# Kernel tuning notes

Measured on AMD Instinct MI355X. Metric: run time of the kernel, lower is better.

The kernel has to match this reference:

```python
import jax, jax.numpy as jnp
import numpy as np

N_NODES = 50000
N_EDGES = 800000
IN_FEAT = 4
HIDDEN = 128
NUM_LAYERS = 3


def setup_inputs() -> dict:
    key = jax.random.key(0)
    ks = jax.random.split(key, 16)
    x = jax.random.normal(ks[0], (N_NODES, IN_FEAT), dtype=jnp.float32)
    edge_index = jax.random.randint(ks[1], (2, N_EDGES), 0, N_NODES, dtype=jnp.int64)

    def lin(k, fan_in, fan_out):
        bound = 1.0 / np.sqrt(fan_in)
        k1, k2 = jax.random.split(k)
        W = jax.random.uniform(k1, (fan_in, fan_out), minval=-bound, maxval=bound, dtype=jnp.float32)
        b = jax.random.uniform(k2, (fan_out,), minval=-bound, maxval=bound, dtype=jnp.float32)
        return W, b

    W_enc, b_enc = lin(ks[2], IN_FEAT, HIDDEN)
    W_g1, b_g1 = lin(ks[3], HIDDEN, HIDDEN)
    W_g2, b_g2 = lin(ks[4], HIDDEN, HIDDEN)
    W_g3, b_g3 = lin(ks[5], HIDDEN, HIDDEN)
    W_m1, b_m1 = lin(ks[6], 2 * HIDDEN, HIDDEN)
    W_m2, b_m2 = lin(ks[7], HIDDEN, 3)
    return {
        "x": x, "edge_index": edge_index,
        "W_enc": W_enc, "b_enc": b_enc,
        "W_g1": W_g1, "b_g1": b_g1,
        "W_g2": W_g2, "b_g2": b_g2,
        "W_g3": W_g3, "b_g3": b_g3,
        "W_m1": W_m1, "b_m1": b_m1,
        "W_m2": W_m2, "b_m2": b_m2,
    }


def _gcn_forward(x, edge_index, W_enc, b_enc, gcn_params, W_m1, b_m1, W_m2, b_m2):
    n = x.shape[0]
    # Node encoder (linear + ReLU) -> [N, H]
    h = jax.nn.relu(x @ W_enc + b_enc)

    # Add self-loops once (GCNConv default add_self_loops=True)
    src = jnp.concatenate([edge_index[0], jnp.arange(n, dtype=edge_index.dtype)])
    dst = jnp.concatenate([edge_index[1], jnp.arange(n, dtype=edge_index.dtype)])
    # Symmetric degree normalization: D^{-1/2} (A+I) D^{-1/2}
    deg = jax.ops.segment_sum(jnp.ones_like(dst, dtype=h.dtype), dst, num_segments=n)
    deg_inv_sqrt = jnp.where(deg > 0, jax.lax.rsqrt(jnp.maximum(deg, 1.0)), 0.0)
    norm = (deg_inv_sqrt[src] * deg_inv_sqrt[dst])[:, None]  # [E+N, 1]

    for (W, b) in gcn_params:
        m = (h @ W)[src] * norm                       # gather + scale messages
        h = jax.ops.segment_sum(m, dst, num_segments=n) + b
        h = jax.nn.relu(h)                            # dropout is identity at eval

    # Edge classifier: gather endpoints, concat, MLP -> [E, 3]
    ef = jnp.concatenate([h[edge_index[0]], h[edge_index[1]]], axis=-1)
    return jax.nn.relu(ef @ W_m1 + b_m1) @ W_m2 + b_m2


def reference(x, edge_index, W_enc, b_enc, W_g1, b_g1, W_g2, b_g2, W_g3, b_g3, W_m1, b_m1, W_m2, b_m2):
    gcn_params = [(W_g1, b_g1), (W_g2, b_g2), (W_g3, b_g3)]
    return _gcn_forward(x, edge_index, W_enc, b_enc, gcn_params, W_m1, b_m1, W_m2, b_m2)
```

## Files before the change

### kernel.cpp

```cpp
#include <hip/hip_runtime.h>
#include <hip/hip_bf16.h>

#define N_NODES 50000
#define N_EDGES 800000
#define HID 128
#define SCAN_BLK 512
#define N_SCAN_BLOCKS ((N_NODES + SCAN_BLK - 1) / SCAN_BLK)

typedef __attribute__((ext_vector_type(8))) short bf16x8;
typedef __attribute__((ext_vector_type(4))) float f32x4;

__device__ __forceinline__ ushort f2bf(float f) {
    uint u = __float_as_uint(f);
    return (ushort)((u + 0x7FFFu + ((u >> 16) & 1u)) >> 16);
}
__device__ __forceinline__ float bf2f(ushort h) { return __uint_as_float(((uint)h) << 16); }

__global__ void k_count(const int* __restrict__ ei, int* cnt) {
    int e = blockIdx.x * blockDim.x + threadIdx.x;
    if (e < N_EDGES) atomicAdd(&cnt[ei[N_EDGES + e]], 1);
}

__global__ __launch_bounds__(SCAN_BLK) void k_scan1(const int* __restrict__ cnt,
                                                    int* __restrict__ rowStart,
                                                    int* __restrict__ blockSums,
                                                    float* __restrict__ dinv) {
    __shared__ int tmp[SCAN_BLK];
    int i = blockIdx.x * SCAN_BLK + threadIdx.x;
    int v = (i < N_NODES) ? cnt[i] : 0;
    if (i < N_NODES) dinv[i] = rsqrtf(1.0f + (float)v);
    tmp[threadIdx.x] = v;
    __syncthreads();
    for (int off = 1; off < SCAN_BLK; off <<= 1) {
        int t = (threadIdx.x >= off) ? tmp[threadIdx.x - off] : 0;
        __syncthreads();
        tmp[threadIdx.x] += t;
        __syncthreads();
    }
    if (i < N_NODES) rowStart[i] = tmp[threadIdx.x] - v;
    if (threadIdx.x == SCAN_BLK - 1) blockSums[blockIdx.x] = tmp[SCAN_BLK - 1];
}

__global__ __launch_bounds__(SCAN_BLK) void k_scan23(int* __restrict__ rowStart,
                                                     const int* __restrict__ blockSums,
                                                     int* __restrict__ cursor) {
    __shared__ int ps[128];
    int t = threadIdx.x;
    if (t < 128) ps[t] = (t < N_SCAN_BLOCKS) ? blockSums[t] : 0;
    __syncthreads();
    for (int off = 1; off < 128; off <<= 1) {
        int v = (t < 128 && t >= off) ? ps[t - off] : 0;
        __syncthreads();
        if (t < 128) ps[t] += v;
        __syncthreads();
    }
    int i = blockIdx.x * SCAN_BLK + t;
    int prefix = (blockIdx.x == 0) ? 0 : ps[blockIdx.x - 1];
    if (i < N_NODES) {
        rowStart[i] += prefix;
        cursor[i] = 0;
    }
    if (i == 0) rowStart[N_NODES] = N_EDGES;
}

__global__ void k_fill(const int* __restrict__ ei, const int* __restrict__ rowStart,
                       int* cursor, int2* __restrict__ csrE) {
    int e = blockIdx.x * blockDim.x + threadIdx.x;
    if (e < N_EDGES) {
        int s = ei[e];
        int d = ei[N_EDGES + e];
        int pos = rowStart[d] + atomicAdd(&cursor[d], 1);
        csrE[pos] = make_int2(s, e);
    }
}

struct WSplitArgs {
    const float* src[5];
    ushort* th[5];
    ushort* tl[5];
};

__global__ void k_tsplit5(WSplitArgs a) {
    int i = blockIdx.x * 256 + threadIdx.x;
    int which = i >> 14, r = i & 16383;
    int k = r >> 7, j = r & 127;
    float v = a.src[which][r];
    ushort hi = f2bf(v);
    a.th[which][j * 128 + k] = hi;
    a.tl[which][j * 128 + k] = f2bf(v - bf2f(hi));
}

__global__ void k_encoder(const float* __restrict__ x, const float* __restrict__ W,
                          const float* __restrict__ b, ushort* __restrict__ hH,
                          ushort* __restrict__ hL) {
    int i = blockIdx.x * 256 + threadIdx.x;
    int n = i >> 6, l = i & 63;
    int j = l * 2;
    float4 xv = *(const float4*)(x + (size_t)n * 4);
    float2 acc = *(const float2*)(b + j);
    float2 w0 = *(const float2*)(W + 0 * 128 + j);
    float2 w1 = *(const float2*)(W + 1 * 128 + j);
    float2 w2 = *(const float2*)(W + 2 * 128 + j);
    float2 w3 = *(const float2*)(W + 3 * 128 + j);
    acc.x += xv.x * w0.x + xv.y * w1.x + xv.z * w2.x + xv.w * w3.x;
    acc.y += xv.x * w0.y + xv.y * w1.y + xv.z * w2.y + xv.w * w3.y;
    float v0 = fmaxf(acc.x, 0.f), v1 = fmaxf(acc.y, 0.f);
    ushort h0 = f2bf(v0), h1 = f2bf(v1);
    ushort l0 = f2bf(v0 - bf2f(h0)), l1 = f2bf(v1 - bf2f(h1));
    ((uint*)hH)[i] = (uint)h0 | ((uint)h1 << 16);
    ((uint*)hL)[i] = (uint)l0 | ((uint)l1 << 16);
}

__global__ __launch_bounds__(256) void k_gemm_mfma(const ushort* __restrict__ AH,
                                                   const ushort* __restrict__ AL,
                                                   const ushort* __restrict__ BTH,
                                                   const ushort* __restrict__ BTL,
                                                   float* __restrict__ out,
                                                   const float* __restrict__ scale, int M) {
    int tid = threadIdx.x;
    int w = tid >> 6, l = tid & 63;
    int ln = l & 15, lk = l >> 4;
    int r0 = blockIdx.x * 128 + w * 32;
    int row0 = r0 + ln, row1 = r0 + 16 + ln;
    int a0 = row0 < M ? row0 : M - 1;
    int a1 = row1 < M ? row1 : M - 1;

    f32x4 acc0[8] = {};
    f32x4 acc1[8] = {};
#pragma unroll
    for (int kc = 0; kc < 4; ++kc) {
        int ko = kc * 32 + lk * 8;
        bf16x8 h0H = *(const bf16x8*)(AH + (size_t)a0 * 128 + ko);
        bf16x8 h0L = *(const bf16x8*)(AL + (size_t)a0 * 128 + ko);
        bf16x8 h1H = *(const bf16x8*)(AH + (size_t)a1 * 128 + ko);
        bf16x8 h1L = *(const bf16x8*)(AL + (size_t)a1 * 128 + ko);
#pragma unroll
        for (int nt = 0; nt < 8; ++nt) {
            size_t boff = (size_t)(nt * 16 + ln) * 128 + ko;
            bf16x8 wH = *(const bf16x8*)(BTH + boff);
            bf16x8 wL = *(const bf16x8*)(BTL + boff);
            acc0[nt] = __builtin_amdgcn_mfma_f32_16x16x32_bf16(wH, h0H, acc0[nt], 0, 0, 0);
            acc0[nt] = __builtin_amdgcn_mfma_f32_16x16x32_bf16(wL, h0H, acc0[nt], 0, 0, 0);
            acc0[nt] = __builtin_amdgcn_mfma_f32_16x16x32_bf16(wH, h0L, acc0[nt], 0, 0, 0);
            acc1[nt] = __builtin_amdgcn_mfma_f32_16x16x32_bf16(wH, h1H, acc1[nt], 0, 0, 0);
            acc1[nt] = __builtin_amdgcn_mfma_f32_16x16x32_bf16(wL, h1H, acc1[nt], 0, 0, 0);
            acc1[nt] = __builtin_amdgcn_mfma_f32_16x16x32_bf16(wH, h1L, acc1[nt], 0, 0, 0);
        }
    }
    float s0v = scale[a0];
    float s1v = scale[a1];
#pragma unroll
    for (int nt = 0; nt < 8; ++nt) {
        int jb = nt * 16 + lk * 4;
        if (row0 < M) {
            float4 o = make_float4(acc0[nt][0] * s0v, acc0[nt][1] * s0v,
                                   acc0[nt][2] * s0v, acc0[nt][3] * s0v);
            *(float4*)(out + (size_t)row0 * 128 + jb) = o;
        }
        if (row1 < M) {
            float4 o = make_float4(acc1[nt][0] * s1v, acc1[nt][1] * s1v,
                                   acc1[nt][2] * s1v, acc1[nt][3] * s1v);
            *(float4*)(out + (size_t)row1 * 128 + jb) = o;
        }
    }
}

__global__ __launch_bounds__(512, 8) void k_agg_gemm(
    const float* __restrict__ hw, const float* __restrict__ bg,
    const float* __restrict__ dinv, const int* __restrict__ rowStart,
    const int2* __restrict__ csrE,
    const ushort* __restrict__ BTH1, const ushort* __restrict__ BTL1,
    const ushort* __restrict__ BTH2, const ushort* __restrict__ BTL2,
    float* __restrict__ out1, float* __restrict__ out2,
    const float* __restrict__ b1, const float* __restrict__ outScale) {
    __shared__ uint AsH[16][64];
    __shared__ uint AsL[16][64];
    int tid = threadIdx.x;
    int w = tid >> 6, l = tid & 63;
    int g = l >> 4, li = l & 15;
    int c8 = li * 8;

#pragma unroll
    for (int q = 0; q < 2; ++q) {
        int n = blockIdx.x * 16 + w * 2 + q;
        float4 aA, aB;
        if (g == 0) {
            aA = *(const float4*)(hw + (size_t)n * 128 + c8);
            aB = *(const float4*)(hw + (size_t)n * 128 + c8 + 4);
        } else {
            aA = make_float4(0.f, 0.f, 0.f, 0.f);
            aB = aA;
        }
        int s0 = rowStart[n], s1 = rowStart[n + 1];
        int k = s0 + g;
        float4 v0a = make_float4(0.f, 0.f, 0.f, 0.f), v0b = v0a;
        if (k < s1) {
            const float* r = hw + (size_t)csrE[k].x * 128 + c8;
            v0a = *(const float4*)(r);
            v0b = *(const float4*)(r + 4);
        }
        for (; k < s1; k += 4) {
            float4 v1a = make_float4(0.f, 0.f, 0.f, 0.f), v1b = v1a;
            if (k + 4 < s1) {
                const float* r = hw + (size_t)csrE[k + 4].x * 128 + c8;
                v1a = *(const float4*)(r);
                v1b = *(const float4*)(r + 4);
            }
            aA.x += v0a.x; aA.y += v0a.y; aA.z += v0a.z; aA.w += v0a.w;
            aB.x += v0b.x; aB.y += v0b.y; aB.z += v0b.z; aB.w += v0b.w;
            v0a = v1a;
            v0b = v1b;
        }
        aA.x += __shfl_xor(aA.x, 16); aA.y += __shfl_xor(aA.y, 16);
        aA.z += __shfl_xor(aA.z, 16); aA.w += __shfl_xor(aA.w, 16);
        aB.x += __shfl_xor(aB.x, 16); aB.y += __shfl_xor(aB.y, 16);
        aB.z += __shfl_xor(aB.z, 16); aB.w += __shfl_xor(aB.w, 16);
        aA.x += __shfl_xor(aA.x, 32); aA.y += __shfl_xor(aA.y, 32);
        aA.z += __shfl_xor(aA.z, 32); aA.w += __shfl_xor(aA.w, 32);
        aB.x += __shfl_xor(aB.x, 32); aB.y += __shfl_xor(aB.y, 32);
        aB.z += __shfl_xor(aB.z, 32); aB.w += __shfl_xor(aB.w, 32);

        if (g == 0) {
            float di = dinv[n];
            float4 bbA = *(const float4*)(bg + c8);
            float4 bbB = *(const float4*)(bg + c8 + 4);
            float f0 = fmaxf(bbA.x + di * aA.x, 0.f);
            float f1 = fmaxf(bbA.y + di * aA.y, 0.f);
            float f2 = fmaxf(bbA.z + di * aA.z, 0.f);
            float f3 = fmaxf(bbA.w + di * aA.w, 0.f);
            float f4 = fmaxf(bbB.x + di * aB.x, 0.f);
            float f5 = fmaxf(bbB.y + di * aB.y, 0.f);
            float f6 = fmaxf(bbB.z + di * aB.z, 0.f);
            float f7 = fmaxf(bbB.w + di * aB.w, 0.f);
            ushort h0 = f2bf(f0), h1 = f2bf(f1), h2 = f2bf(f2), h3 = f2bf(f3);
            ushort h4 = f2bf(f4), h5 = f2bf(f5), h6 = f2bf(f6), h7 = f2bf(f7);
            uint4 uh = make_uint4((uint)h0 | ((uint)h1 << 16), (uint)h2 | ((uint)h3 << 16),
                                  (uint)h4 | ((uint)h5 << 16), (uint)h6 | ((uint)h7 << 16));
            ushort l0 = f2bf(f0 - bf2f(h0)), l1 = f2bf(f1 - bf2f(h1));
            ushort l2 = f2bf(f2 - bf2f(h2)), l3 = f2bf(f3 - bf2f(h3));
            ushort l4 = f2bf(f4 - bf2f(h4)), l5 = f2bf(f5 - bf2f(h5));
            ushort l6 = f2bf(f6 - bf2f(h6)), l7 = f2bf(f7 - bf2f(h7));
            uint4 ul = make_uint4((uint)l0 | ((uint)l1 << 16), (uint)l2 | ((uint)l3 << 16),
                                  (uint)l4 | ((uint)l5 << 16), (uint)l6 | ((uint)l7 << 16));
            int r = w * 2 + q;
            *(uint4*)&AsH[r][li * 4] = uh;
            *(uint4*)&AsL[r][li * 4] = ul;
        }
    }
    __syncthreads();

    int ln = l & 15, lk = l >> 4;
    int ct = w;
    int node = blockIdx.x * 16 + ln;
    f32x4 acc1 = {};
    f32x4 acc2 = {};
#pragma unroll
    for (int kc = 0; kc < 4; ++kc) {
        uint4 uh = *(uint4*)&AsH[ln][kc * 16 + lk * 4];
        uint4 ul = *(uint4*)&AsL[ln][kc * 16 + lk * 4];
        bf16x8 hh, hl;
        __builtin_memcpy(&hh, &uh, 16);
        __builtin_memcpy(&hl, &ul, 16);
        size_t boff = (size_t)(ct * 16 + ln) * 128 + kc * 32 + lk * 8;
        bf16x8 wh = *(const bf16x8*)(BTH1 + boff);
        bf16x8 wl = *(const bf16x8*)(BTL1 + boff);
        acc1 = __builtin_amdgcn_mfma_f32_16x16x32_bf16(wh, hh, acc1, 0, 0, 0);
        acc1 = __builtin_amdgcn_mfma_f32_16x16x32_bf16(wl, hh, acc1, 0, 0, 0);
        acc1 = __builtin_amdgcn_mfma_f32_16x16x32_bf16(wh, hl, acc1, 0, 0, 0);
        if (BTH2) {
            bf16x8 wh2 = *(const bf16x8*)(BTH2 + boff);
            bf16x8 wl2 = *(const bf16x8*)(BTL2 + boff);
            acc2 = __builtin_amdgcn_mfma_f32_16x16x32_bf16(wh2, hh, acc2, 0, 0, 0);
            acc2 = __builtin_amdgcn_mfma_f32_16x16x32_bf16(wl2, hh, acc2, 0, 0, 0);
            acc2 = __builtin_amdgcn_mfma_f32_16x16x32_bf16(wh2, hl, acc2, 0, 0, 0);
        }
    }
    int jb = ct * 16 + lk * 4;
    if (outScale) {
        float s = outScale[node];
        *(float4*)(out1 + (size_t)node * 128 + jb) =
            make_float4(acc1[0] * s, acc1[1] * s, acc1[2] * s, acc1[3] * s);
    } else {
        *(float4*)(out1 + (size_t)node * 128 + jb) =
            make_float4(acc1[0], acc1[1], acc1[2], acc1[3]);
        float4 bv = *(const float4*)(b1 + jb);
        *(float4*)(out2 + (size_t)node * 128 + jb) =
            make_float4(acc2[0] + bv.x, acc2[1] + bv.y, acc2[2] + bv.z, acc2[3] + bv.w);
    }
}

__global__ __launch_bounds__(256) void k_edge_final(const float* __restrict__ P,
                                                    const float* __restrict__ Qb,
                                                    const int* __restrict__ rowStart,
                                                    const int2* __restrict__ csrE,
                                                    const float* __restrict__ W2,
                                                    const float* __restrict__ b2,
                                                    float* __restrict__ out) {
    int wid = (blockIdx.x * 256 + threadIdx.x) >> 6;
    int l = threadIdx.x & 63;
    if (wid >= N_NODES) return;
    int s0 = rowStart[wid], s1 = rowStart[wid + 1];
    if (s0 >= s1) return;
    int j8 = (l & 15) * 8;
    int g = l >> 4;

    float4 qa = *(const float4*)(Qb + (size_t)wid * 128 + j8);
    float4 qb = *(const float4*)(Qb + (size_t)wid * 128 + j8 + 4);
    float w2r[8][3];
#pragma unroll
    for (int k = 0; k < 8; ++k) {
        w2r[k][0] = W2[(j8 + k) * 3 + 0];
        w2r[k][1] = W2[(j8 + k) * 3 + 1];
        w2r[k][2] = W2[(j8 + k) * 3 + 2];
    }
    float bz0 = b2[0], bz1 = b2[1], bz2 = b2[2];

    int k = s0 + g;
    int2 c = make_int2(0, 0);
    float4 pa = make_float4(0.f, 0.f, 0.f, 0.f), pb = pa;
    if (k < s1) {
        c = csrE[k];
        const float* pr = P + (size_t)c.x * 128 + j8;
        pa = *(const float4*)(pr);
        pb = *(const float4*)(pr + 4);
    }
    for (; k < s1; k += 4) {
        int kn = k + 4;
        int2 cn = make_int2(0, 0);
        float4 pan = make_float4(0.f, 0.f, 0.f, 0.f), pbn = pan;
        if (kn < s1) {
            cn = csrE[kn];
            const float* prn = P + (size_t)cn.x * 128 + j8;
            pan = *(const float4*)(prn);
            pbn = *(const float4*)(prn + 4);
        }
        float z[8];
        z[0] = fmaxf(pa.x + qa.x, 0.f);
        z[1] = fmaxf(pa.y + qa.y, 0.f);
        z[2] = fmaxf(pa.z + qa.z, 0.f);
        z[3] = fmaxf(pa.w + qa.w, 0.f);
        z[4] = fmaxf(pb.x + qb.x, 0.f);
        z[5] = fmaxf(pb.y + qb.y, 0.f);
        z[6] = fmaxf(pb.z + qb.z, 0.f);
        z[7] = fmaxf(pb.w + qb.w, 0.f);
        float o0 = 0.f, o1 = 0.f, o2 = 0.f;
#pragma unroll
        for (int q = 0; q < 8; ++q) {
            o0 += z[q] * w2r[q][0];
            o1 += z[q] * w2r[q][1];
            o2 += z[q] * w2r[q][2];
        }
#pragma unroll
        for (int m = 1; m < 16; m <<= 1) {
            o0 += __shfl_xor(o0, m);
            o1 += __shfl_xor(o1, m);
            o2 += __shfl_xor(o2, m);
        }
        if ((l & 15) == 0) {
            float* op = out + (size_t)c.y * 3;
            op[0] = o0 + bz0;
            op[1] = o1 + bz1;
            op[2] = o2 + bz2;
        }
        c = cn;
        pa = pan;
        pb = pbn;
    }
}

extern "C" void kernel_launch(void* const* d_in, const int* in_sizes, int n_in,
                              void* d_out, int out_size, void* d_ws, size_t ws_size,
                              hipStream_t stream) {
    const float* x     = (const float*)d_in[0];
    const int*   ei    = (const int*)d_in[1];
    const float* W_enc = (const float*)d_in[2];
    const float* b_enc = (const float*)d_in[3];
    const float* Wg[3] = {(const float*)d_in[4], (const float*)d_in[6], (const float*)d_in[8]};
    const float* bg[3] = {(const float*)d_in[5], (const float*)d_in[7], (const float*)d_in[9]};
    const float* W_m1  = (const float*)d_in[10];
    const float* b_m1  = (const float*)d_in[11];
    const float* W_m2  = (const float*)d_in[12];
    const float* b_m2  = (const float*)d_in[13];
    float* out = (float*)d_out;

    char* w = (char*)d_ws;
    ushort* hH      = (ushort*)w;  w += (size_t)N_NODES * HID * 2;
    ushort* hL      = (ushort*)w;  w += (size_t)N_NODES * HID * 2;
    float*  bufA    = (float*)w;   w += (size_t)N_NODES * HID * 4;
    float*  bufB    = (float*)w;   w += (size_t)N_NODES * HID * 4;
    int2*   csrE    = (int2*)w;    w += (size_t)N_EDGES * 8;
    float*  dinv    = (float*)w;   w += (size_t)N_NODES * 4;
    int*    rowStart= (int*)w;     w += (size_t)(N_NODES + 4) * 4;
    int*    cursor  = (int*)w;     w += (size_t)N_NODES * 4;
    int*    blockSums=(int*)w;     w += 512;
    ushort* WgTH[3], *WgTL[3];
    for (int i = 0; i < 3; ++i) {
        WgTH[i] = (ushort*)w; w += 128 * 128 * 2;
        WgTL[i] = (ushort*)w; w += 128 * 128 * 2;
    }
    ushort* WtTH = (ushort*)w; w += 128 * 128 * 2;
    ushort* WtTL = (ushort*)w; w += 128 * 128 * 2;
    ushort* WbTH = (ushort*)w; w += 128 * 128 * 2;
    ushort* WbTL = (ushort*)w; w += 128 * 128 * 2;

    float* P  = (float*)hH;
    float* Qb = bufB;

    hipMemsetAsync(cursor, 0, (size_t)N_NODES * 4, stream);
    k_count<<<(N_EDGES + 255) / 256, 256, 0, stream>>>(ei, cursor);
    k_scan1<<<N_SCAN_BLOCKS, SCAN_BLK, 0, stream>>>(cursor, rowStart, blockSums, dinv);
    k_scan23<<<N_SCAN_BLOCKS, SCAN_BLK, 0, stream>>>(rowStart, blockSums, cursor);
    k_fill<<<(N_EDGES + 255) / 256, 256, 0, stream>>>(ei, rowStart, cursor, csrE);

    WSplitArgs wa;
    wa.src[0] = Wg[0]; wa.th[0] = WgTH[0]; wa.tl[0] = WgTL[0];
    wa.src[1] = Wg[1]; wa.th[1] = WgTH[1]; wa.tl[1] = WgTL[1];
    wa.src[2] = Wg[2]; wa.th[2] = WgTH[2]; wa.tl[2] = WgTL[2];
    wa.src[3] = W_m1;             wa.th[3] = WtTH; wa.tl[3] = WtTL;
    wa.src[4] = W_m1 + 128 * 128; wa.th[4] = WbTH; wa.tl[4] = WbTL;
    k_tsplit5<<<5 * 16384 / 256, 256, 0, stream>>>(wa);

    k_encoder<<<N_NODES * 64 / 256, 256, 0, stream>>>(x, W_enc, b_enc, hH, hL);

    k_gemm_mfma<<<(N_NODES + 127) / 128, 256, 0, stream>>>(hH, hL, WgTH[0], WgTL[0], bufA, dinv, N_NODES);

    const int fusedGrid = N_NODES / 16;
    k_agg_gemm<<<fusedGrid, 512, 0, stream>>>(bufA, bg[0], dinv, rowStart, csrE,
                                              WgTH[1], WgTL[1], nullptr, nullptr,
                                              bufB, nullptr, nullptr, dinv);
    k_agg_gemm<<<fusedGrid, 512, 0, stream>>>(bufB, bg[1], dinv, rowStart, csrE,
                                              WgTH[2], WgTL[2], nullptr, nullptr,
                                              bufA, nullptr, nullptr, dinv);
    k_agg_gemm<<<fusedGrid, 512, 0, stream>>>(bufA, bg[2], dinv, rowStart, csrE,
                                              WtTH, WtTL, WbTH, WbTL,
                                              P, Qb, b_m1, nullptr);

    k_edge_final<<<(N_NODES * 64) / 256, 256, 0, stream>>>(P, Qb, rowStart, csrE, W_m2, b_m2, out);
}
```

Before: 477.3 us.

## Renumber nodes by in-degree so aggregation blocks get balanced neighbor counts

Replaces the CSR prefix scan with a degree-bucket histogram and ranking pass that permutes nodes so that consecutive nodes have equal in-degree. The encoder writes features in permuted order, and the CSR stores permuted source indices. The aggregation kernel now gives two nodes to each wavefront, using half-waves of two lanes per feature group, and pads the shared-memory rows to avoid bank conflicts. The goal is less wavefront divergence and load imbalance from uneven degrees during the gather loops. The cost is extra preprocessing kernels, and the locality of the random gathers changes. The final edge output still appears to be indexed by the original edge id.

```diff
diff --git a/kernel.cpp b/kernel.cpp
--- a/kernel.cpp
+++ b/kernel.cpp
@@ -4,8 +4,8 @@
 #define N_NODES 50000
 #define N_EDGES 800000
 #define HID 128
-#define SCAN_BLK 512
-#define N_SCAN_BLOCKS ((N_NODES + SCAN_BLK - 1) / SCAN_BLK)
+#define NBUCKET 1024
+#define N_NODE_BLOCKS ((N_NODES + 255) / 256)
 
 typedef __attribute__((ext_vector_type(8))) short bf16x8;
 typedef __attribute__((ext_vector_type(4))) float f32x4;
@@ -21,56 +21,80 @@
     if (e < N_EDGES) atomicAdd(&cnt[ei[N_EDGES + e]], 1);
 }
 
-__global__ __launch_bounds__(SCAN_BLK) void k_scan1(const int* __restrict__ cnt,
-                                                    int* __restrict__ rowStart,
-                                                    int* __restrict__ blockSums,
-                                                    float* __restrict__ dinv) {
-    __shared__ int tmp[SCAN_BLK];
-    int i = blockIdx.x * SCAN_BLK + threadIdx.x;
-    int v = (i < N_NODES) ? cnt[i] : 0;
-    if (i < N_NODES) dinv[i] = rsqrtf(1.0f + (float)v);
-    tmp[threadIdx.x] = v;
+__global__ __launch_bounds__(256) void k_bhist(const int* __restrict__ cnt, int* gHist,
+                                               int* __restrict__ blockBase) {
+    __shared__ int lh[NBUCKET];
+    int t = threadIdx.x;
+    for (int d = t; d < NBUCKET; d += 256) lh[d] = 0;
     __syncthreads();
-    for (int off = 1; off < SCAN_BLK; off <<= 1) {
-        int t = (threadIdx.x >= off) ? tmp[threadIdx.x - off] : 0;
+    int n = blockIdx.x * 256 + t;
+    if (n < N_NODES) {
+        int deg = min(cnt[n], NBUCKET - 1);
+        atomicAdd(&lh[deg], 1);
+    }
+    __syncthreads();
+    for (int d = t; d < NBUCKET; d += 256) {
+        int c = lh[d];
+        blockBase[blockIdx.x * NBUCKET + d] = c ? atomicAdd(&gHist[d], c) : 0;
+    }
+}
+
+__global__ __launch_bounds__(NBUCKET) void k_prefix(const int* __restrict__ gHist,
+                                                    int* __restrict__ histBase,
+                                                    int* __restrict__ edgeBase,
+                                                    int* __restrict__ rowStartP) {
+    __shared__ int a[NBUCKET];
+    __shared__ int b[NBUCKET];
+    int t = threadIdx.x;
+    int h = gHist[t];
+    a[t] = h;
+    b[t] = h * t;
+    __syncthreads();
+    for (int off = 1; off < NBUCKET; off <<= 1) {
+        int av = (t >= off) ? a[t - off] : 0;
+        int bv = (t >= off) ? b[t - off] : 0;
         __syncthreads();
-        tmp[threadIdx.x] += t;
+        a[t] += av;
+        b[t] += bv;
         __syncthreads();
     }
-    if (i < N_NODES) rowStart[i] = tmp[threadIdx.x] - v;
-    if (threadIdx.x == SCAN_BLK - 1) blockSums[blockIdx.x] = tmp[SCAN_BLK - 1];
-}
-
-__global__ __launch_bounds__(SCAN_BLK) void k_scan23(int* __restrict__ rowStart,
-                                                     const int* __restrict__ blockSums,
-                                                     int* __restrict__ cursor) {
-    __shared__ int ps[128];
+    histBase[t] = a[t] - h;
+    edgeBase[t] = b[t] - h * t;
+    if (t == 0) rowStartP[N_NODES] = N_EDGES;
+}
+
+__global__ __launch_bounds__(256) void k_rank(const int* __restrict__ cnt,
+                                              const int* __restrict__ histBase,
+                                              const int* __restrict__ edgeBase,
+                                              const int* __restrict__ blockBase,
+                                              int* __restrict__ rank,
+                                              int* __restrict__ rowStartP,
+                                              float* __restrict__ dinvP) {
+    __shared__ int cur[NBUCKET];
     int t = threadIdx.x;
-    if (t < 128) ps[t] = (t < N_SCAN_BLOCKS) ? blockSums[t] : 0;
+    for (int d = t; d < NBUCKET; d += 256) cur[d] = 0;
     __syncthreads();
-    for (int off = 1; off < 128; off <<= 1) {
-        int v = (t < 128 && t >= off) ? ps[t - off] : 0;
-        __syncthreads();
-        if (t < 128) ps[t] += v;
-        __syncthreads();
-    }
-    int i = blockIdx.x * SCAN_BLK + t;
-    int prefix = (blockIdx.x == 0) ? 0 : ps[blockIdx.x - 1];
-    if (i < N_NODES) {
-        rowStart[i] += prefix;
-        cursor[i] = 0;
-    }
-    if (i == 0) rowStart[N_NODES] = N_EDGES;
-}
-
-__global__ void k_fill(const int* __restrict__ ei, const int* __restrict__ rowStart,
-                       int* cursor, int2* __restrict__ csrE) {
+    int n = blockIdx.x * 256 + t;
+    if (n < N_NODES) {
+        int deg = min(cnt[n], NBUCKET - 1);
+        int slot = atomicAdd(&cur[deg], 1);
+        int r = histBase[deg] + blockBase[blockIdx.x * NBUCKET + deg] + slot;
+        rank[n] = r;
+        rowStartP[r] = edgeBase[deg] + (r - histBase[deg]) * deg;
+        dinvP[r] = rsqrtf(1.0f + (float)deg);
+    }
+}
+
+__global__ void k_fill(const int* __restrict__ ei, const int* __restrict__ rank,
+                       const int* __restrict__ rowStartP, int* cursorP,
+                       int2* __restrict__ csrE) {
     int e = blockIdx.x * blockDim.x + threadIdx.x;
     if (e < N_EDGES) {
         int s = ei[e];
         int d = ei[N_EDGES + e];
-        int pos = rowStart[d] + atomicAdd(&cursor[d], 1);
-        csrE[pos] = make_int2(s, e);
+        int rd = rank[d];
+        int pos = rowStartP[rd] + atomicAdd(&cursorP[rd], 1);
+        csrE[pos] = make_int2(rank[s], e);
     }
 }
 
@@ -91,8 +115,8 @@
 }
 
 __global__ void k_encoder(const float* __restrict__ x, const float* __restrict__ W,
-                          const float* __restrict__ b, ushort* __restrict__ hH,
-                          ushort* __restrict__ hL) {
+                          const float* __restrict__ b, const int* __restrict__ rank,
+                          ushort* __restrict__ hH, ushort* __restrict__ hL) {
     int i = blockIdx.x * 256 + threadIdx.x;
     int n = i >> 6, l = i & 63;
     int j = l * 2;
@@ -107,8 +131,9 @@
     float v0 = fmaxf(acc.x, 0.f), v1 = fmaxf(acc.y, 0.f);
     ushort h0 = f2bf(v0), h1 = f2bf(v1);
     ushort l0 = f2bf(v0 - bf2f(h0)), l1 = f2bf(v1 - bf2f(h1));
-    ((uint*)hH)[i] = (uint)h0 | ((uint)h1 << 16);
-    ((uint*)hL)[i] = (uint)l0 | ((uint)l1 << 16);
+    size_t o = (size_t)rank[n] * 64 + l;
+    ((uint*)hH)[o] = (uint)h0 | ((uint)h1 << 16);
+    ((uint*)hL)[o] = (uint)l0 | ((uint)l1 << 16);
 }
 
 __global__ __launch_bounds__(256) void k_gemm_mfma(const ushort* __restrict__ AH,
@@ -153,99 +178,92 @@
     for (int nt = 0; nt < 8; ++nt) {
         int jb = nt * 16 + lk * 4;
         if (row0 < M) {
-            float4 o = make_float4(acc0[nt][0] * s0v, acc0[nt][1] * s0v,
-                                   acc0[nt][2] * s0v, acc0[nt][3] * s0v);
-            *(float4*)(out + (size_t)row0 * 128 + jb) = o;
+            *(float4*)(out + (size_t)row0 * 128 + jb) =
+                make_float4(acc0[nt][0] * s0v, acc0[nt][1] * s0v, acc0[nt][2] * s0v, acc0[nt][3] * s0v);
         }
         if (row1 < M) {
-            float4 o = make_float4(acc1[nt][0] * s1v, acc1[nt][1] * s1v,
-                                   acc1[nt][2] * s1v, acc1[nt][3] * s1v);
-            *(float4*)(out + (size_t)row1 * 128 + jb) = o;
+            *(float4*)(out + (size_t)row1 * 128 + jb) =
+                make_float4(acc1[nt][0] * s1v, acc1[nt][1] * s1v, acc1[nt][2] * s1v, acc1[nt][3] * s1v);
         }
     }
 }
 
 __global__ __launch_bounds__(512, 8) void k_agg_gemm(
     const float* __restrict__ hw, const float* __restrict__ bg,
-    const float* __restrict__ dinv, const int* __restrict__ rowStart,
+    const float* __restrict__ dinvP, const int* __restrict__ rowStartP,
     const int2* __restrict__ csrE,
     const ushort* __restrict__ BTH1, const ushort* __restrict__ BTL1,
     const ushort* __restrict__ BTH2, const ushort* __restrict__ BTL2,
     float* __restrict__ out1, float* __restrict__ out2,
     const float* __restrict__ b1, const float* __restrict__ outScale) {
-    __shared__ uint AsH[16][64];
-    __shared__ uint AsL[16][64];
+    __shared__ uint AsH[16][68];
+    __shared__ uint AsL[16][68];
     int tid = threadIdx.x;
     int w = tid >> 6, l = tid & 63;
-    int g = l >> 4, li = l & 15;
+    int sub = l >> 5;
+    int g2 = (l >> 4) & 1;
+    int li = l & 15;
     int c8 = li * 8;
-
-#pragma unroll
-    for (int q = 0; q < 2; ++q) {
-        int n = blockIdx.x * 16 + w * 2 + q;
-        float4 aA, aB;
-        if (g == 0) {
-            aA = *(const float4*)(hw + (size_t)n * 128 + c8);
-            aB = *(const float4*)(hw + (size_t)n * 128 + c8 + 4);
-        } else {
-            aA = make_float4(0.f, 0.f, 0.f, 0.f);
-            aB = aA;
-        }
-        int s0 = rowStart[n], s1 = rowStart[n + 1];
-        int k = s0 + g;
-        float4 v0a = make_float4(0.f, 0.f, 0.f, 0.f), v0b = v0a;
-        if (k < s1) {
-            const float* r = hw + (size_t)csrE[k].x * 128 + c8;
-            v0a = *(const float4*)(r);
-            v0b = *(const float4*)(r + 4);
-        }
-        for (; k < s1; k += 4) {
-            float4 v1a = make_float4(0.f, 0.f, 0.f, 0.f), v1b = v1a;
-            if (k + 4 < s1) {
-                const float* r = hw + (size_t)csrE[k + 4].x * 128 + c8;
-                v1a = *(const float4*)(r);
-                v1b = *(const float4*)(r + 4);
-            }
-            aA.x += v0a.x; aA.y += v0a.y; aA.z += v0a.z; aA.w += v0a.w;
-            aB.x += v0b.x; aB.y += v0b.y; aB.z += v0b.z; aB.w += v0b.w;
-            v0a = v1a;
-            v0b = v1b;
-        }
-        aA.x += __shfl_xor(aA.x, 16); aA.y += __shfl_xor(aA.y, 16);
-        aA.z += __shfl_xor(aA.z, 16); aA.w += __shfl_xor(aA.w, 16);
-        aB.x += __shfl_xor(aB.x, 16); aB.y += __shfl_xor(aB.y, 16);
-        aB.z += __shfl_xor(aB.z, 16); aB.w += __shfl_xor(aB.w, 16);
-        aA.x += __shfl_xor(aA.x, 32); aA.y += __shfl_xor(aA.y, 32);
-        aA.z += __shfl_xor(aA.z, 32); aA.w += __shfl_xor(aA.w, 32);
-        aB.x += __shfl_xor(aB.x, 32); aB.y += __shfl_xor(aB.y, 32);
-        aB.z += __shfl_xor(aB.z, 32); aB.w += __shfl_xor(aB.w, 32);
-
-        if (g == 0) {
-            float di = dinv[n];
-            float4 bbA = *(const float4*)(bg + c8);
-            float4 bbB = *(const float4*)(bg + c8 + 4);
-            float f0 = fmaxf(bbA.x + di * aA.x, 0.f);
-            float f1 = fmaxf(bbA.y + di * aA.y, 0.f);
-            float f2 = fmaxf(bbA.z + di * aA.z, 0.f);
-            float f3 = fmaxf(bbA.w + di * aA.w, 0.f);
-            float f4 = fmaxf(bbB.x + di * aB.x, 0.f);
-            float f5 = fmaxf(bbB.y + di * aB.y, 0.f);
-            float f6 = fmaxf(bbB.z + di * aB.z, 0.f);
-            float f7 = fmaxf(bbB.w + di * aB.w, 0.f);
-            ushort h0 = f2bf(f0), h1 = f2bf(f1), h2 = f2bf(f2), h3 = f2bf(f3);
-            ushort h4 = f2bf(f4), h5 = f2bf(f5), h6 = f2bf(f6), h7 = f2bf(f7);
-            uint4 uh = make_uint4((uint)h0 | ((uint)h1 << 16), (uint)h2 | ((uint)h3 << 16),
-                                  (uint)h4 | ((uint)h5 << 16), (uint)h6 | ((uint)h7 << 16));
-            ushort l0 = f2bf(f0 - bf2f(h0)), l1 = f2bf(f1 - bf2f(h1));
-            ushort l2 = f2bf(f2 - bf2f(h2)), l3 = f2bf(f3 - bf2f(h3));
-            ushort l4 = f2bf(f4 - bf2f(h4)), l5 = f2bf(f5 - bf2f(h5));
-            ushort l6 = f2bf(f6 - bf2f(h6)), l7 = f2bf(f7 - bf2f(h7));
-            uint4 ul = make_uint4((uint)l0 | ((uint)l1 << 16), (uint)l2 | ((uint)l3 << 16),
-                                  (uint)l4 | ((uint)l5 << 16), (uint)l6 | ((uint)l7 << 16));
-            int r = w * 2 + q;
-            *(uint4*)&AsH[r][li * 4] = uh;
-            *(uint4*)&AsL[r][li * 4] = ul;
-        }
+    int n = blockIdx.x * 16 + w * 2 + sub;
+
+    float4 aA, aB;
+    if (g2 == 0) {
+        aA = *(const float4*)(hw + (size_t)n * 128 + c8);
+        aB = *(const float4*)(hw + (size_t)n * 128 + c8 + 4);
+    } else {
+        aA = make_float4(0.f, 0.f, 0.f, 0.f);
+        aB = aA;
+    }
+    int s0 = rowStartP[n], s1 = rowStartP[n + 1];
+    int k = s0 + g2;
+    float4 v0a = make_float4(0.f, 0.f, 0.f, 0.f), v0b = v0a;
+    if (k < s1) {
+        const float* r = hw + (size_t)csrE[k].x * 128 + c8;
+        v0a = *(const float4*)(r);
+        v0b = *(const float4*)(r + 4);
+    }
+    for (; k < s1; k += 2) {
+        float4 v1a = make_float4(0.f, 0.f, 0.f, 0.f), v1b = v1a;
+        if (k + 2 < s1) {
+            const float* r = hw + (size_t)csrE[k + 2].x * 128 + c8;
+            v1a = *(const float4*)(r);
+            v1b = *(const float4*)(r + 4);
+        }
+        aA.x += v0a.x; aA.y += v0a.y; aA.z += v0a.z; aA.w += v0a.w;
+        aB.x += v0b.x; aB.y += v0b.y; aB.z += v0b.z; aB.w += v0b.w;
+        v0a = v1a;
+        v0b = v1b;
+    }
+    aA.x += __shfl_xor(aA.x, 16); aA.y += __shfl_xor(aA.y, 16);
+    aA.z += __shfl_xor(aA.z, 16); aA.w += __shfl_xor(aA.w, 16);
+    aB.x += __shfl_xor(aB.x, 16); aB.y += __shfl_xor(aB.y, 16);
+    aB.z += __shfl_xor(aB.z, 16); aB.w += __shfl_xor(aB.w, 16);
+
+    if (g2 == 0) {
+        float di = dinvP[n];
+        float4 bbA = *(const float4*)(bg + c8);
+        float4 bbB = *(const float4*)(bg + c8 + 4);
+        float f0 = fmaxf(bbA.x + di * aA.x, 0.f);
+        float f1 = fmaxf(bbA.y + di * aA.y, 0.f);
+        float f2 = fmaxf(bbA.z + di * aA.z, 0.f);
+        float f3 = fmaxf(bbA.w + di * aA.w, 0.f);
+        float f4 = fmaxf(bbB.x + di * aB.x, 0.f);
+        float f5 = fmaxf(bbB.y + di * aB.y, 0.f);
+        float f6 = fmaxf(bbB.z + di * aB.z, 0.f);
+        float f7 = fmaxf(bbB.w + di * aB.w, 0.f);
+        ushort h0 = f2bf(f0), h1 = f2bf(f1), h2 = f2bf(f2), h3 = f2bf(f3);
+        ushort h4 = f2bf(f4), h5 = f2bf(f5), h6 = f2bf(f6), h7 = f2bf(f7);
+        uint4 uh = make_uint4((uint)h0 | ((uint)h1 << 16), (uint)h2 | ((uint)h3 << 16),
+                              (uint)h4 | ((uint)h5 << 16), (uint)h6 | ((uint)h7 << 16));
+        ushort l0 = f2bf(f0 - bf2f(h0)), l1 = f2bf(f1 - bf2f(h1));
+        ushort l2 = f2bf(f2 - bf2f(h2)), l3 = f2bf(f3 - bf2f(h3));
+        ushort l4 = f2bf(f4 - bf2f(h4)), l5 = f2bf(f5 - bf2f(h5));
+        ushort l6 = f2bf(f6 - bf2f(h6)), l7 = f2bf(f7 - bf2f(h7));
+        uint4 ul = make_uint4((uint)l0 | ((uint)l1 << 16), (uint)l2 | ((uint)l3 << 16),
+                              (uint)l4 | ((uint)l5 << 16), (uint)l6 | ((uint)l7 << 16));
+        int r = w * 2 + sub;
+        *(uint4*)&AsH[r][li * 4] = uh;
+        *(uint4*)&AsL[r][li * 4] = ul;
     }
     __syncthreads();
 
@@ -291,7 +309,7 @@
 
 __global__ __launch_bounds__(256) void k_edge_final(const float* __restrict__ P,
                                                     const float* __restrict__ Qb,
-                                                    const int* __restrict__ rowStart,
+                                                    const int* __restrict__ rowStartP,
                                                     const int2* __restrict__ csrE,
                                                     const float* __restrict__ W2,
                                                     const float* __restrict__ b2,
@@ -299,7 +317,7 @@
     int wid = (blockIdx.x * 256 + threadIdx.x) >> 6;
     int l = threadIdx.x & 63;
     if (wid >= N_NODES) return;
-    int s0 = rowStart[wid], s1 = rowStart[wid + 1];
+    int s0 = rowStartP[wid], s1 = rowStartP[wid + 1];
     if (s0 >= s1) return;
     int j8 = (l & 15) * 8;
     int g = l >> 4;
@@ -389,10 +407,16 @@
     float*  bufA    = (float*)w;   w += (size_t)N_NODES * HID * 4;
     float*  bufB    = (float*)w;   w += (size_t)N_NODES * HID * 4;
     int2*   csrE    = (int2*)w;    w += (size_t)N_EDGES * 8;
-    float*  dinv    = (float*)w;   w += (size_t)N_NODES * 4;
-    int*    rowStart= (int*)w;     w += (size_t)(N_NODES + 4) * 4;
-    int*    cursor  = (int*)w;     w += (size_t)N_NODES * 4;
-    int*    blockSums=(int*)w;     w += 512;
+    int*    cnt     = (int*)w;     w += (size_t)N_NODES * 4;
+    int*    cursorP = (int*)w;     w += (size_t)N_NODES * 4;
+    int*    gHist   = (int*)w;     w += NBUCKET * 4;
+    size_t  zeroBytes = (size_t)(N_NODES * 2 + NBUCKET) * 4;
+    int*    rank    = (int*)w;     w += (size_t)N_NODES * 4;
+    int*    rowStartP = (int*)w;   w += (size_t)(N_NODES + 4) * 4;
+    float*  dinvP   = (float*)w;   w += (size_t)N_NODES * 4;
+    int*    histBase = (int*)w;    w += NBUCKET * 4;
+    int*    edgeBase = (int*)w;    w += NBUCKET * 4;
+    int*    blockBase = (int*)w;   w += (size_t)N_NODE_BLOCKS * NBUCKET * 4;
     ushort* WgTH[3], *WgTL[3];
     for (int i = 0; i < 3; ++i) {
         WgTH[i] = (ushort*)w; w += 128 * 128 * 2;
@@ -406,11 +430,13 @@
     float* P  = (float*)hH;
     float* Qb = bufB;
 
-    hipMemsetAsync(cursor, 0, (size_t)N_NODES * 4, stream);
-    k_count<<<(N_EDGES + 255) / 256, 256, 0, stream>>>(ei, cursor);
-    k_scan1<<<N_SCAN_BLOCKS, SCAN_BLK, 0, stream>>>(cursor, rowStart, blockSums, dinv);
-    k_scan23<<<N_SCAN_BLOCKS, SCAN_BLK, 0, stream>>>(rowStart, blockSums, cursor);
-    k_fill<<<(N_EDGES + 255) / 256, 256, 0, stream>>>(ei, rowStart, cursor, csrE);
+    hipMemsetAsync(cnt, 0, zeroBytes, stream);
+    k_count<<<(N_EDGES + 255) / 256, 256, 0, stream>>>(ei, cnt);
+    k_bhist<<<N_NODE_BLOCKS, 256, 0, stream>>>(cnt, gHist, blockBase);
+    k_prefix<<<1, NBUCKET, 0, stream>>>(gHist, histBase, edgeBase, rowStartP);
+    k_rank<<<N_NODE_BLOCKS, 256, 0, stream>>>(cnt, histBase, edgeBase, blockBase,
+                                              rank, rowStartP, dinvP);
+    k_fill<<<(N_EDGES + 255) / 256, 256, 0, stream>>>(ei, rank, rowStartP, cursorP, csrE);
 
     WSplitArgs wa;
     wa.src[0] = Wg[0]; wa.th[0] = WgTH[0]; wa.tl[0] = WgTL[0];
@@ -420,20 +446,22 @@
     wa.src[4] = W_m1 + 128 * 128; wa.th[4] = WbTH; wa.tl[4] = WbTL;
     k_tsplit5<<<5 * 16384 / 256, 256, 0, stream>>>(wa);
 
-    k_encoder<<<N_NODES * 64 / 256, 256, 0, stream>>>(x, W_enc, b_enc, hH, hL);
-
-    k_gemm_mfma<<<(N_NODES + 127) / 128, 256, 0, stream>>>(hH, hL, WgTH[0], WgTL[0], bufA, dinv, N_NODES);
+    k_encoder<<<N_NODES * 64 / 256, 256, 0, stream>>>(x, W_enc, b_enc, rank, hH, hL);
+
+    k_gemm_mfma<<<(N_NODES + 127) / 128, 256, 0, stream>>>(hH, hL, WgTH[0], WgTL[0],
+                                                           bufA, dinvP, N_NODES);
 
     const int fusedGrid = N_NODES / 16;
-    k_agg_gemm<<<fusedGrid, 512, 0, stream>>>(bufA, bg[0], dinv, rowStart, csrE,
+    k_agg_gemm<<<fusedGrid, 512, 0, stream>>>(bufA, bg[0], dinvP, rowStartP, csrE,
                                               WgTH[1], WgTL[1], nullptr, nullptr,
-                                              bufB, nullptr, nullptr, dinv);
-    k_agg_gemm<<<fusedGrid, 512, 0, stream>>>(bufB, bg[1], dinv, rowStart, csrE,
+                                              bufB, nullptr, nullptr, dinvP);
+    k_agg_gemm<<<fusedGrid, 512, 0, stream>>>(bufB, bg[1], dinvP, rowStartP, csrE,
                                               WgTH[2], WgTL[2], nullptr, nullptr,
-                                              bufA, nullptr, nullptr, dinv);
-    k_agg_gemm<<<fusedGrid, 512, 0, stream>>>(bufA, bg[2], dinv, rowStart, csrE,
+                                              bufA, nullptr, nullptr, dinvP);
+    k_agg_gemm<<<fusedGrid, 512, 0, stream>>>(bufA, bg[2], dinvP, rowStartP, csrE,
                                               WtTH, WtTL, WbTH, WbTL,
                                               P, Qb, b_m1, nullptr);
 
-    k_edge_final<<<(N_NODES * 64) / 256, 256, 0, stream>>>(P, Qb, rowStart, csrE, W_m2, b_m2, out);
-}
+    k_edge_final<<<(N_NODES * 64) / 256, 256, 0, stream>>>(P, Qb, rowStartP, csrE,
+                                                           W_m2, b_m2, out);
+}
```

After: 456.8 us. -4.3%, faster.
